# Kernel tuning notes

Hardware: AMD Instinct MI355X
Metric: run time of the kernel (lower is better)

## Reference

```python
import jax, jax.numpy as jnp
import numpy as np

DIM = 512
NUM_HEADS = 8
HEAD_DIM = DIM // NUM_HEADS
LN_EPS = 1e-5


def setup_inputs() -> dict:
    key = jax.random.key(0)
    k1, k2, k3 = jax.random.split(key, 3)
    x = jax.random.normal(k1, (8, DIM, 32, 32), dtype=jnp.float32)
    # torch Linear default init scale ~ 1/sqrt(fan_in); keep values sane
    w_qkv = jax.random.normal(k2, (3 * DIM, DIM), dtype=jnp.float32) * (DIM ** -0.5)
    b_qkv = jax.random.normal(k3, (3 * DIM,), dtype=jnp.float32) * 0.01
    ln_gamma = jnp.ones((DIM,), dtype=jnp.float32)
    ln_beta = jnp.zeros((DIM,), dtype=jnp.float32)
    return {"x": x, "w_qkv": w_qkv, "b_qkv": b_qkv, "ln_gamma": ln_gamma, "ln_beta": ln_beta}


def _rotate_half(t):
    t1, t2 = jnp.split(t, 2, axis=-1)
    return jnp.concatenate((-t2, t1), axis=-1)


def reference(x, w_qkv, b_qkv, ln_gamma, ln_beta):
    B, C, H, W = x.shape
    N = H * W
    nh, hd = NUM_HEADS, HEAD_DIM
    scale = hd ** -0.5

    # [B, N, C]
    xt = x.reshape(B, C, N).transpose(0, 2, 1)

    # LayerNorm over channel dim
    mu = jnp.mean(xt, axis=-1, keepdims=True)
    var = jnp.mean(jnp.square(xt - mu), axis=-1, keepdims=True)
    xn = (xt - mu) * jax.lax.rsqrt(var + LN_EPS) * ln_gamma + ln_beta

    # QKV projection: [B, N, 3C]
    qkv = xn @ w_qkv.T + b_qkv
    qkv = qkv.reshape(B, N, 3, nh, hd).transpose(2, 0, 3, 1, 4)  # [3, B, nh, N, hd]
    q, k, v = qkv[0], qkv[1], qkv[2]

    # RoPE tables
    freqs = 1.0 / (10000.0 ** (jnp.arange(0, hd, 2, dtype=jnp.float32) / hd))
    pos = jnp.arange(N, dtype=jnp.float32)
    sinusoid = jnp.einsum('i,j->ij', pos, freqs)  # [N, hd/2]
    sin = jnp.repeat(jnp.sin(sinusoid), 2, axis=-1)[None, None]  # [1,1,N,hd]
    cos = jnp.repeat(jnp.cos(sinusoid), 2, axis=-1)[None, None]

    q = q * cos + _rotate_half(q) * sin
    k = k * cos + _rotate_half(k) * sin

    # Full softmax attention: [B, nh, N, N]
    attn = jnp.einsum('bhqd,bhkd->bhqk', q, k) * scale
    attn = jax.nn.softmax(attn, axis=-1)
    out = jnp.einsum('bhqk,bhkd->bhqd', attn, v)  # [B, nh, N, hd]

    out = out.transpose(0, 2, 1, 3).reshape(B, N, C)  # [B, N, C]
    # dropout=0 (eval): identity
    return out.transpose(0, 2, 1).reshape(B, C, H, W)
```

## Files before the change

### kernel.cpp

```cpp
#include <hip/hip_runtime.h>
#include <hip/hip_bf16.h>
#include <math.h>

using bf16 = __hip_bfloat16;
typedef __attribute__((ext_vector_type(8))) short short8;
typedef __attribute__((ext_vector_type(4))) float floatx4;
typedef __attribute__((ext_vector_type(4))) unsigned int uint4_;
typedef __attribute__((ext_vector_type(2))) unsigned int uint2_;

#define C_DIM   512
#define N_TOK   1024
#define NHEAD   8
#define HDIM    64
#define LN_EPSF 1e-5f

__device__ __forceinline__ unsigned short f2b(float f) {
    union { float f; unsigned int u; } v; v.f = f;
    unsigned int r = v.u + 0x7FFFu + ((v.u >> 16) & 1u);
    return (unsigned short)(r >> 16);
}
__device__ __forceinline__ float b2f(unsigned short u) {
    union { unsigned int i; float f; } v; v.i = ((unsigned int)u) << 16; return v.f;
}
__device__ __forceinline__ unsigned int cvt_pk_bf16(float lo, float hi) {
    unsigned int r;
    asm("v_cvt_pk_bf16_f32 %0, %1, %2" : "=v"(r) : "v"(lo), "v"(hi));
    return r;
}
__device__ __forceinline__ float fast_exp2(float x) {
    return __builtin_amdgcn_exp2f(x);
}

__global__ __launch_bounds__(256) void prep_kernel(
        const float* __restrict__ x, const float* __restrict__ w,
        float* __restrict__ mu, float* __restrict__ rsig,
        float* __restrict__ sc, unsigned short* __restrict__ wf) {
    __shared__ float red_s[4][64];
    __shared__ float red_q[4][64];
    const int bx = blockIdx.x;
    const int t  = threadIdx.x;
    if (bx < 128) {
        const int rl = t & 63;
        const int cg = t >> 6;
        const int r0 = bx * 64;
        const int b  = r0 >> 10;
        const int n  = (r0 & 1023) + rl;
        const float* xp = x + (size_t)b * C_DIM * N_TOK + n;
        float s = 0.f, q = 0.f;
        #pragma unroll 4
        for (int i = 0; i < 128; ++i) {
            float v = xp[(size_t)(cg * 128 + i) * N_TOK];
            s += v; q += v * v;
        }
        red_s[cg][rl] = s; red_q[cg][rl] = q;
        __syncthreads();
        if (cg == 0) {
            float S = red_s[0][rl] + red_s[1][rl] + red_s[2][rl] + red_s[3][rl];
            float Q = red_q[0][rl] + red_q[1][rl] + red_q[2][rl] + red_q[3][rl];
            float m   = S * (1.0f / C_DIM);
            float var = Q * (1.0f / C_DIM) - m * m;
            mu[r0 + rl]   = m;
            rsig[r0 + rl] = rsqrtf(var + LN_EPSF);
        }
    } else if (bx < 256) {
        const int idx = (bx - 128) * 256 + t;
        const int n = idx >> 5, f = idx & 31;
        const float fr = __expf((float)f * (-9.210340371976184f / 32.0f));
        float sv, cv;
        sincosf((float)n * fr, &sv, &cv);
        ((float2*)sc)[idx] = make_float2(sv, cv);
    } else {
        const int id   = (bx - 256) * 256 + t;
        const int lane = id & 63;
        const int ksl  = (id >> 6) & 15;
        const int j16  = id >> 10;
        const int c    = lane & 15;
        const int quad = lane >> 4;
        const float* wp = w + (size_t)(j16 * 16 + c) * C_DIM + ksl * 32 + quad * 8;
        const float4 w0 = *(const float4*)(wp);
        const float4 w1 = *(const float4*)(wp + 4);
        uint4_ pk;
        pk.x = cvt_pk_bf16(w0.x, w0.y);
        pk.y = cvt_pk_bf16(w0.z, w0.w);
        pk.z = cvt_pk_bf16(w1.x, w1.y);
        pk.w = cvt_pk_bf16(w1.z, w1.w);
        *(uint4_*)(wf + (size_t)id * 8) = pk;
    }
}

__global__ __launch_bounds__(256) void xnt_kernel(
        const float* __restrict__ x, const float* __restrict__ gamma,
        const float* __restrict__ beta, const float* __restrict__ mu,
        const float* __restrict__ rsig, unsigned short* __restrict__ xnf) {
    __shared__ short Sx[64][72];
    const int t  = threadIdx.x;
    const int c0 = blockIdx.x * 64;
    const int n0 = blockIdx.y * 64;
    const int b  = blockIdx.z;

    const int nq  = t & 15;
    const int crl = t >> 4;
    const int tok = b * N_TOK + n0 + nq * 4;
    const float4 m4 = *(const float4*)(mu + tok);
    const float4 r4 = *(const float4*)(rsig + tok);
    #pragma unroll
    for (int p = 0; p < 4; ++p) {
        const int c = c0 + p * 16 + crl;
        const float g = gamma[c], bt = beta[c];
        const float4 xv = *(const float4*)(x + (size_t)b * C_DIM * N_TOK + (size_t)c * N_TOK + n0 + nq * 4);
        Sx[nq * 4 + 0][p * 16 + crl] = (short)f2b((xv.x - m4.x) * r4.x * g + bt);
        Sx[nq * 4 + 1][p * 16 + crl] = (short)f2b((xv.y - m4.y) * r4.y * g + bt);
        Sx[nq * 4 + 2][p * 16 + crl] = (short)f2b((xv.z - m4.z) * r4.z * g + bt);
        Sx[nq * 4 + 3][p * 16 + crl] = (short)f2b((xv.w - m4.w) * r4.w * g + bt);
    }
    __syncthreads();
    const int wv   = t >> 6;
    const int lane = t & 63;
    const int cfr  = lane & 15;
    const int quad = lane >> 4;
    const int g16  = b * 64 + ((n0 >> 4) + wv);
    #pragma unroll
    for (int ks = 0; ks < 2; ++ks) {
        short8 v = *(const short8*)&Sx[wv * 16 + cfr][ks * 32 + quad * 8];
        *(short8*)(xnf + (((size_t)g16 * 16 + (c0 >> 5) + ks) * 64 + lane) * 8) = v;
    }
}

__global__ __launch_bounds__(256) void qkv_mfma_kernel(
        const unsigned short* __restrict__ xnf, const unsigned short* __restrict__ wf,
        const float* __restrict__ bias, const float* __restrict__ sc,
        unsigned short* __restrict__ qfr, unsigned short* __restrict__ kfr,
        unsigned short* __restrict__ vfr) {
    __shared__ short Es[4][64][72];

    const int t    = threadIdx.x;
    const int wv   = t >> 6;
    const int lane = t & 63;
    const int cl   = lane & 15;
    const int quad = lane >> 4;
    const int t0   = blockIdx.x * 128 + (wv & 1) * 64;
    const int j0w  = blockIdx.y * 128 + (wv >> 1) * 64;
    const int which = j0w >> 9;
    const int h     = (j0w >> 6) & 7;
    const int b     = t0 >> 10;
    const int n0q   = t0 & 1023;
    const int bh    = b * NHEAD + h;

    const unsigned short* ap = xnf + (size_t)(t0 >> 4) * 8192 + lane * 8;
    const unsigned short* bp = wf  + (size_t)(j0w >> 4) * 8192 + lane * 8;

    floatx4 acc[4][4];
    #pragma unroll
    for (int i = 0; i < 4; ++i)
        #pragma unroll
        for (int j = 0; j < 4; ++j) acc[i][j] = (floatx4){0.f, 0.f, 0.f, 0.f};

    #pragma unroll 2
    for (int kt = 0; kt < 16; ++kt) {
        short8 af[4], bfr[4];
        #pragma unroll
        for (int tt = 0; tt < 4; ++tt) af[tt]  = *(const short8*)(ap + ((size_t)tt * 16 + kt) * 512);
        #pragma unroll
        for (int jt = 0; jt < 4; ++jt) bfr[jt] = *(const short8*)(bp + ((size_t)jt * 16 + kt) * 512);
        #pragma unroll
        for (int tt = 0; tt < 4; ++tt)
            #pragma unroll
            for (int jt = 0; jt < 4; ++jt)
                acc[tt][jt] = __builtin_amdgcn_mfma_f32_16x16x32_bf16(af[tt], bfr[jt], acc[tt][jt], 0, 0, 0);
    }

    const float os = (which == 0) ? 0.125f : 1.0f;
    float bj[4];
    #pragma unroll
    for (int jt = 0; jt < 4; ++jt) bj[jt] = bias[j0w + jt * 16 + cl] * os;
    #pragma unroll
    for (int tt = 0; tt < 4; ++tt)
        #pragma unroll
        for (int jt = 0; jt < 4; ++jt)
            #pragma unroll
            for (int r = 0; r < 4; ++r)
                Es[wv][tt * 16 + quad * 4 + r][jt * 16 + cl] = (short)f2b(fmaf(acc[tt][jt][r], os, bj[jt]));

    if (which == 2) {
        unsigned short* vfb = vfr + ((size_t)bh * 16 + (n0q >> 6)) * 4096;
        #pragma unroll
        for (int dt = 0; dt < 4; ++dt) {
            #pragma unroll
            for (int ks = 0; ks < 2; ++ks) {
                short8 pk;
                #pragma unroll
                for (int j = 0; j < 8; ++j)
                    pk[j] = Es[wv][ks * 32 + quad * 8 + j][dt * 16 + cl];
                *(short8*)(vfb + (((size_t)dt * 2 + ks) * 64 + lane) * 8) = pk;
            }
        }
    } else {
        unsigned short* base = (which == 0)
            ? qfr + ((size_t)bh * 64 + (n0q >> 4)) * 1024
            : kfr + ((size_t)bh * 16 + (n0q >> 6)) * 4096;
        #pragma unroll
        for (int mt = 0; mt < 4; ++mt) {
            const int n = n0q + mt * 16 + cl;
            const float* scp = sc + ((size_t)n * 32 + quad * 4) * 2;
            #pragma unroll
            for (int ks = 0; ks < 2; ++ks) {
                const short8 v8 = *(const short8*)&Es[wv][mt * 16 + cl][ks * 32 + quad * 8];
                const short8 p8 = *(const short8*)&Es[wv][mt * 16 + cl][(ks ^ 1) * 32 + quad * 8];
                const float* sp = scp + ks * 32;
                const float4 s0 = *(const float4*)sp;
                const float4 s1 = *(const float4*)(sp + 4);
                const float sv[4] = {s0.x, s0.z, s1.x, s1.z};
                const float cv[4] = {s0.y, s0.w, s1.y, s1.w};
                const float sgn = ks ? 1.0f : -1.0f;
                uint4_ pk;
                unsigned int pw[4];
                #pragma unroll
                for (int f = 0; f < 4; ++f) {
                    const float svs = sgn * sv[f];
                    const float a0 = b2f((unsigned short)v8[2 * f]);
                    const float a1 = b2f((unsigned short)v8[2 * f + 1]);
                    const float p0 = b2f((unsigned short)p8[2 * f]);
                    const float p1 = b2f((unsigned short)p8[2 * f + 1]);
                    pw[f] = cvt_pk_bf16(fmaf(p0, svs, a0 * cv[f]),
                                        fmaf(p1, svs, a1 * cv[f]));
                }
                pk.x = pw[0]; pk.y = pw[1]; pk.z = pw[2]; pk.w = pw[3];
                *(uint4_*)(base + (((size_t)mt * 2 + ks) * 64 + lane) * 8) = pk;
            }
        }
    }
}

__global__ __launch_bounds__(256, 2) void attn_mfma_kernel(
        const unsigned short* __restrict__ qfr, const unsigned short* __restrict__ kfr,
        const unsigned short* __restrict__ vfr, float* __restrict__ out) {
    __shared__ __align__(16) short Plds[4][2][16][72];

    const int t    = threadIdx.x;
    const int wv   = t >> 6;
    const int lane = t & 63;
    const int c    = lane & 15;
    const int quad = lane >> 4;
    const int i    = blockIdx.x;
    const int bh   = (i & 7) * 8 + ((i >> 3) & 7);
    const int q32  = (i >> 6) * 4 + wv;
    const int b    = bh >> 3, h = bh & 7;

    const unsigned short* qp   = qfr + ((size_t)bh * 64 + q32 * 2) * 1024 + lane * 8;
    const unsigned short* kraw = kfr + (size_t)bh * 65536 + lane * 8;
    const unsigned short* vraw = vfr + (size_t)bh * 65536 + lane * 8;

    short8 qf[2][2];
    qf[0][0] = *(const short8*)(qp);
    qf[0][1] = *(const short8*)(qp + 512);
    qf[1][0] = *(const short8*)(qp + 1024);
    qf[1][1] = *(const short8*)(qp + 1536);

    floatx4 o_acc[4][2];
    float l_acc[2] = {0.f, 0.f};
    #pragma unroll
    for (int dt = 0; dt < 4; ++dt) {
        o_acc[dt][0] = (floatx4){0.f, 0.f, 0.f, 0.f};
        o_acc[dt][1] = (floatx4){0.f, 0.f, 0.f, 0.f};
    }

    const float LOG2E  = 1.4426950408889634f;
    const float ESHIFT = -23.083120654223414f;

    short8 kfA[4][2], vfA[4][2], kfB[4][2], vfB[4][2];

    auto loadf = [&](short8 (&kf)[4][2], short8 (&vf)[4][2], int kt) {
        const unsigned short* kc = kraw + (size_t)kt * 4096;
        const unsigned short* vc = vraw + (size_t)kt * 4096;
        #pragma unroll
        for (int mt = 0; mt < 4; ++mt)
            #pragma unroll
            for (int ks = 0; ks < 2; ++ks) {
                kf[mt][ks] = *(const short8*)(kc + (mt * 2 + ks) * 512);
                vf[mt][ks] = *(const short8*)(vc + (mt * 2 + ks) * 512);
            }
    };

    auto step = [&](short8 (&kf)[4][2], short8 (&vf)[4][2]) {
        floatx4 st[4][2];
        __builtin_amdgcn_s_setprio(1);
        #pragma unroll
        for (int mt = 0; mt < 4; ++mt)
            #pragma unroll
            for (int u = 0; u < 2; ++u) {
                floatx4 z = (floatx4){0.f, 0.f, 0.f, 0.f};
                z = __builtin_amdgcn_mfma_f32_16x16x32_bf16(kf[mt][0], qf[u][0], z, 0, 0, 0);
                st[mt][u] = __builtin_amdgcn_mfma_f32_16x16x32_bf16(kf[mt][1], qf[u][1], z, 0, 0, 0);
            }
        __builtin_amdgcn_s_setprio(0);

        #pragma unroll
        for (int u = 0; u < 2; ++u)
            #pragma unroll
            for (int mt = 0; mt < 4; ++mt) {
                const float e0 = fast_exp2(fmaf(st[mt][u][0], LOG2E, ESHIFT));
                const float e1 = fast_exp2(fmaf(st[mt][u][1], LOG2E, ESHIFT));
                const float e2 = fast_exp2(fmaf(st[mt][u][2], LOG2E, ESHIFT));
                const float e3 = fast_exp2(fmaf(st[mt][u][3], LOG2E, ESHIFT));
                l_acc[u] += (e0 + e1) + (e2 + e3);
                uint2_ pk;
                pk.x = cvt_pk_bf16(e0, e1);
                pk.y = cvt_pk_bf16(e2, e3);
                *(uint2_*)&Plds[wv][u][c][mt * 16 + quad * 4] = pk;
            }

        #pragma unroll
        for (int u = 0; u < 2; ++u) {
            const short8 pf0 = *(const short8*)&Plds[wv][u][c][quad * 8];
            const short8 pf1 = *(const short8*)&Plds[wv][u][c][32 + quad * 8];
            __builtin_amdgcn_s_setprio(1);
            #pragma unroll
            for (int dt = 0; dt < 4; ++dt) {
                o_acc[dt][u] = __builtin_amdgcn_mfma_f32_16x16x32_bf16(vf[dt][0], pf0, o_acc[dt][u], 0, 0, 0);
                o_acc[dt][u] = __builtin_amdgcn_mfma_f32_16x16x32_bf16(vf[dt][1], pf1, o_acc[dt][u], 0, 0, 0);
            }
            __builtin_amdgcn_s_setprio(0);
        }
    };

    loadf(kfA, vfA, 0);
    #pragma unroll 1
    for (int kt = 0; kt < 16; kt += 2) {
        loadf(kfB, vfB, kt + 1);
        step(kfA, vfA);
        if (kt + 2 < 16) loadf(kfA, vfA, kt + 2);
        step(kfB, vfB);
    }

    #pragma unroll
    for (int u = 0; u < 2; ++u) {
        float l = l_acc[u];
        l += __shfl_xor(l, 16);
        l += __shfl_xor(l, 32);
        const float inv = 1.0f / l;
        const int qcol = (q32 * 2 + u) * 16 + c;
        #pragma unroll
        for (int dt = 0; dt < 4; ++dt)
            #pragma unroll
            for (int r = 0; r < 4; ++r) {
                const int d = dt * 16 + quad * 4 + r;
                out[((size_t)b * C_DIM + h * HDIM + d) * N_TOK + qcol] = o_acc[dt][u][r] * inv;
            }
    }
}

extern "C" void kernel_launch(void* const* d_in, const int* in_sizes, int n_in,
                              void* d_out, int out_size, void* d_ws, size_t ws_size,
                              hipStream_t stream) {
    const float* x     = (const float*)d_in[0];
    const float* w     = (const float*)d_in[1];
    const float* bias  = (const float*)d_in[2];
    const float* gamma = (const float*)d_in[3];
    const float* beta  = (const float*)d_in[4];
    float* out = (float*)d_out;

    char* ws = (char*)d_ws;
    float* mu   = (float*)ws;
    float* rsig = (float*)(ws + 32768);
    unsigned short* qfr = (unsigned short*)(ws + 65536);
    unsigned short* kfr = (unsigned short*)(ws + 65536 + 8388608);
    unsigned short* vfr = (unsigned short*)(ws + 65536 + 16777216);
    unsigned short* xnf = (unsigned short*)(ws + 65536 + 25165824);
    unsigned short* wf  = (unsigned short*)(ws + 65536 + 33554432);
    float* sc           = (float*)(ws + 65536 + 35127296);

    hipLaunchKernelGGL(prep_kernel, dim3(640), dim3(256), 0, stream, x, w, mu, rsig, sc, wf);
    hipLaunchKernelGGL(xnt_kernel, dim3(8, 16, 8), dim3(256), 0, stream,
                       x, gamma, beta, mu, rsig, xnf);
    hipLaunchKernelGGL(qkv_mfma_kernel, dim3(64, 12), dim3(256), 0, stream,
                       xnf, wf, bias, sc, qfr, kfr, vfr);
    hipLaunchKernelGGL(attn_mfma_kernel, dim3(512), dim3(256), 0, stream, qfr, kfr, vfr, out);
}
```

Before: 139.0 us.

## Fuse LayerNorm statistics and normalization into one kernel with LDS-staged tile

Merges the separate LayerNorm-statistics pass and the normalize/transpose pass into a single kernel. Each block stages a 512-channel by 32-token tile of x in shared memory, computes mean and rstd there, and writes the bf16 MFMA-fragment layout directly. This removes one kernel launch, a second full read of x, and the mu/rsig round trip through global memory. In exchange it uses about 72KB of LDS per block, which lowers occupancy, and the shared-memory column reads may cause bank conflicts.

```diff
diff --git a/kernel.cpp b/kernel.cpp
--- a/kernel.cpp
+++ b/kernel.cpp
@@ -31,46 +31,90 @@
     return __builtin_amdgcn_exp2f(x);
 }
 
-__global__ __launch_bounds__(256) void prep_kernel(
+__global__ __launch_bounds__(256) void lnx_kernel(
         const float* __restrict__ x, const float* __restrict__ w,
-        float* __restrict__ mu, float* __restrict__ rsig,
-        float* __restrict__ sc, unsigned short* __restrict__ wf) {
-    __shared__ float red_s[4][64];
-    __shared__ float red_q[4][64];
+        const float* __restrict__ gamma, const float* __restrict__ beta,
+        float* __restrict__ sc, unsigned short* __restrict__ wf,
+        unsigned short* __restrict__ xnf) {
+    __shared__ float xs[C_DIM][36];
+    __shared__ float red_s[8][32];
+    __shared__ float red_q[8][32];
+    __shared__ float muL[32], rsL[32];
+
     const int bx = blockIdx.x;
     const int t  = threadIdx.x;
-    if (bx < 128) {
-        const int rl = t & 63;
-        const int cg = t >> 6;
-        const int r0 = bx * 64;
-        const int b  = r0 >> 10;
-        const int n  = (r0 & 1023) + rl;
-        const float* xp = x + (size_t)b * C_DIM * N_TOK + n;
+
+    if (bx < 256) {
+        const int b  = bx >> 5;
+        const int n0 = (bx & 31) * 32;
+        const float* xb = x + (size_t)b * C_DIM * N_TOK;
+
+        #pragma unroll
+        for (int i = 0; i < 16; ++i) {
+            const int flat = i * 256 + t;
+            const int c  = flat >> 3;
+            const int f4 = flat & 7;
+            const float4 v = *(const float4*)(xb + (size_t)c * N_TOK + n0 + f4 * 4);
+            *(float4*)&xs[c][f4 * 4] = v;
+        }
+        __syncthreads();
+
+        const int tl = t & 31, cg = t >> 5;
         float s = 0.f, q = 0.f;
-        #pragma unroll 4
-        for (int i = 0; i < 128; ++i) {
-            float v = xp[(size_t)(cg * 128 + i) * N_TOK];
+        #pragma unroll 8
+        for (int i2 = 0; i2 < 64; ++i2) {
+            const float v = xs[cg * 64 + i2][tl];
             s += v; q += v * v;
         }
-        red_s[cg][rl] = s; red_q[cg][rl] = q;
+        red_s[cg][tl] = s; red_q[cg][tl] = q;
         __syncthreads();
-        if (cg == 0) {
-            float S = red_s[0][rl] + red_s[1][rl] + red_s[2][rl] + red_s[3][rl];
-            float Q = red_q[0][rl] + red_q[1][rl] + red_q[2][rl] + red_q[3][rl];
-            float m   = S * (1.0f / C_DIM);
-            float var = Q * (1.0f / C_DIM) - m * m;
-            mu[r0 + rl]   = m;
-            rsig[r0 + rl] = rsqrtf(var + LN_EPSF);
-        }
-    } else if (bx < 256) {
-        const int idx = (bx - 128) * 256 + t;
+        if (t < 32) {
+            float S = 0.f, Q = 0.f;
+            #pragma unroll
+            for (int g2 = 0; g2 < 8; ++g2) { S += red_s[g2][t]; Q += red_q[g2][t]; }
+            const float m   = S * (1.0f / C_DIM);
+            const float var = Q * (1.0f / C_DIM) - m * m;
+            muL[t] = m; rsL[t] = rsqrtf(var + LN_EPSF);
+        }
+        __syncthreads();
+
+        const int wv   = t >> 6;
+        const int lane = t & 63;
+        const int cfr  = lane & 15;
+        const int quad = lane >> 4;
+        #pragma unroll
+        for (int gg = 0; gg < 2; ++gg) {
+            const int tloc = gg * 16 + cfr;
+            const float m = muL[tloc], r = rsL[tloc];
+            const int g16 = b * 64 + (n0 >> 4) + gg;
+            #pragma unroll
+            for (int kk = 0; kk < 4; ++kk) {
+                const int kt  = wv * 4 + kk;
+                const int ch0 = kt * 32 + quad * 8;
+                const float4 g0 = *(const float4*)(gamma + ch0);
+                const float4 g1 = *(const float4*)(gamma + ch0 + 4);
+                const float4 b0 = *(const float4*)(beta + ch0);
+                const float4 b1 = *(const float4*)(beta + ch0 + 4);
+                float vv[8];
+                #pragma unroll
+                for (int j = 0; j < 8; ++j) vv[j] = (xs[ch0 + j][tloc] - m) * r;
+                uint4_ pk;
+                pk.x = cvt_pk_bf16(vv[0] * g0.x + b0.x, vv[1] * g0.y + b0.y);
+                pk.y = cvt_pk_bf16(vv[2] * g0.z + b0.z, vv[3] * g0.w + b0.w);
+                pk.z = cvt_pk_bf16(vv[4] * g1.x + b1.x, vv[5] * g1.y + b1.y);
+                pk.w = cvt_pk_bf16(vv[6] * g1.z + b1.z, vv[7] * g1.w + b1.w);
+                *(uint4_*)(xnf + (((size_t)g16 * 16 + kt) * 64 + lane) * 8) = pk;
+            }
+        }
+    } else if (bx < 384) {
+        const int idx = (bx - 256) * 256 + t;
         const int n = idx >> 5, f = idx & 31;
         const float fr = __expf((float)f * (-9.210340371976184f / 32.0f));
         float sv, cv;
         sincosf((float)n * fr, &sv, &cv);
         ((float2*)sc)[idx] = make_float2(sv, cv);
     } else {
-        const int id   = (bx - 256) * 256 + t;
+        const int id   = (bx - 384) * 256 + t;
         const int lane = id & 63;
         const int ksl  = (id >> 6) & 15;
         const int j16  = id >> 10;
@@ -85,44 +129,6 @@
         pk.z = cvt_pk_bf16(w1.x, w1.y);
         pk.w = cvt_pk_bf16(w1.z, w1.w);
         *(uint4_*)(wf + (size_t)id * 8) = pk;
-    }
-}
-
-__global__ __launch_bounds__(256) void xnt_kernel(
-        const float* __restrict__ x, const float* __restrict__ gamma,
-        const float* __restrict__ beta, const float* __restrict__ mu,
-        const float* __restrict__ rsig, unsigned short* __restrict__ xnf) {
-    __shared__ short Sx[64][72];
-    const int t  = threadIdx.x;
-    const int c0 = blockIdx.x * 64;
-    const int n0 = blockIdx.y * 64;
-    const int b  = blockIdx.z;
-
-    const int nq  = t & 15;
-    const int crl = t >> 4;
-    const int tok = b * N_TOK + n0 + nq * 4;
-    const float4 m4 = *(const float4*)(mu + tok);
-    const float4 r4 = *(const float4*)(rsig + tok);
-    #pragma unroll
-    for (int p = 0; p < 4; ++p) {
-        const int c = c0 + p * 16 + crl;
-        const float g = gamma[c], bt = beta[c];
-        const float4 xv = *(const float4*)(x + (size_t)b * C_DIM * N_TOK + (size_t)c * N_TOK + n0 + nq * 4);
-        Sx[nq * 4 + 0][p * 16 + crl] = (short)f2b((xv.x - m4.x) * r4.x * g + bt);
-        Sx[nq * 4 + 1][p * 16 + crl] = (short)f2b((xv.y - m4.y) * r4.y * g + bt);
-        Sx[nq * 4 + 2][p * 16 + crl] = (short)f2b((xv.z - m4.z) * r4.z * g + bt);
-        Sx[nq * 4 + 3][p * 16 + crl] = (short)f2b((xv.w - m4.w) * r4.w * g + bt);
-    }
-    __syncthreads();
-    const int wv   = t >> 6;
-    const int lane = t & 63;
-    const int cfr  = lane & 15;
-    const int quad = lane >> 4;
-    const int g16  = b * 64 + ((n0 >> 4) + wv);
-    #pragma unroll
-    for (int ks = 0; ks < 2; ++ks) {
-        short8 v = *(const short8*)&Sx[wv * 16 + cfr][ks * 32 + quad * 8];
-        *(short8*)(xnf + (((size_t)g16 * 16 + (c0 >> 5) + ks) * 64 + lane) * 8) = v;
     }
 }
 
@@ -360,8 +366,6 @@
     float* out = (float*)d_out;
 
     char* ws = (char*)d_ws;
-    float* mu   = (float*)ws;
-    float* rsig = (float*)(ws + 32768);
     unsigned short* qfr = (unsigned short*)(ws + 65536);
     unsigned short* kfr = (unsigned short*)(ws + 65536 + 8388608);
     unsigned short* vfr = (unsigned short*)(ws + 65536 + 16777216);
@@ -369,9 +373,8 @@
     unsigned short* wf  = (unsigned short*)(ws + 65536 + 33554432);
     float* sc           = (float*)(ws + 65536 + 35127296);
 
-    hipLaunchKernelGGL(prep_kernel, dim3(640), dim3(256), 0, stream, x, w, mu, rsig, sc, wf);
-    hipLaunchKernelGGL(xnt_kernel, dim3(8, 16, 8), dim3(256), 0, stream,
-                       x, gamma, beta, mu, rsig, xnf);
+    hipLaunchKernelGGL(lnx_kernel, dim3(768), dim3(256), 0, stream,
+                       x, w, gamma, beta, sc, wf, xnf);
     hipLaunchKernelGGL(qkv_mfma_kernel, dim3(64, 12), dim3(256), 0, stream,
                        xnf, wf, bias, sc, qfr, kfr, vfr);
     hipLaunchKernelGGL(attn_mfma_kernel, dim3(512), dim3(256), 0, stream, qfr, kfr, vfr, out);
```

Result: faster. 125.6 us (-9.6%).
